# Kernel optimization log

Hardware: AMD Instinct MI355X
Metric: run time of the kernel (lower is better)

The kernel has to match this reference:

```python
import jax, jax.numpy as jnp
import numpy as np

B, T, C = 2, 2048, 1024
N_HEAD = 16
HEAD_DIM = C // N_HEAD  # 64


def _apply_rope(x, inv_freq):
    # x: [B, H, T, hd]. Matches the torch module's mixed RoPE variant:
    # cos/sin built from cat(freqs, freqs) but x split by even/odd strides.
    Tn, hd = x.shape[2], x.shape[3]
    t = jnp.arange(Tn, dtype=inv_freq.dtype)
    freqs = t[:, None] * inv_freq[None, :]            # [T, hd/2]
    emb = jnp.concatenate([freqs, freqs], axis=-1)    # [T, hd]
    cos = jnp.cos(emb)[None, None, :, :]
    sin = jnp.sin(emb)[None, None, :, :]
    x1 = x[..., 0::2]
    x2 = x[..., 1::2]
    # interleave (-x2, x1) back to last dim: stack then flatten last two dims
    x_rot = jnp.stack((-x2, x1), axis=-1).reshape(x.shape)
    return x * cos + x_rot * sin


def setup_inputs() -> dict:
    key = jax.random.key(0)
    k1, k2, k3 = jax.random.split(key, 3)
    x = jax.random.normal(k1, (B, T, C), dtype=jnp.float32)
    w_qkv = jax.random.normal(k2, (C, 3 * C), dtype=jnp.float32) * 0.02
    w_proj = jax.random.normal(k3, (C, C), dtype=jnp.float32) * 0.02
    return {"x": x, "w_qkv": w_qkv, "w_proj": w_proj}


def reference(x, w_qkv, w_proj):
    Bn, Tn, Cn = x.shape
    hd = HEAD_DIM
    inv_freq = 1.0 / (10000.0 ** (jnp.arange(0, hd, 2, dtype=jnp.float32) / hd))

    qkv = jnp.einsum('btc,cd->btd', x, w_qkv)  # [B, T, 3C]
    q, k, v = jnp.split(qkv, 3, axis=2)
    # [B, T, C] -> [B, H, T, hd]
    q = q.reshape(Bn, Tn, N_HEAD, hd).transpose(0, 2, 1, 3)
    k = k.reshape(Bn, Tn, N_HEAD, hd).transpose(0, 2, 1, 3)
    v = v.reshape(Bn, Tn, N_HEAD, hd).transpose(0, 2, 1, 3)

    q = _apply_rope(q, inv_freq)
    k = _apply_rope(k, inv_freq)

    scale = 1.0 / jnp.sqrt(jnp.asarray(hd, dtype=q.dtype))
    scores = jnp.einsum('bhqd,bhkd->bhqk', q, k) * scale  # [B, H, T, T]
    causal = jnp.tril(jnp.ones((Tn, Tn), dtype=bool))
    scores = jnp.where(causal[None, None, :, :], scores, -jnp.inf)
    attn = jax.nn.softmax(scores, axis=-1)
    out = jnp.einsum('bhqk,bhkd->bhqd', attn, v)          # [B, H, T, hd]
    y = out.transpose(0, 2, 1, 3).reshape(Bn, Tn, Cn)     # [B, T, C]
    return jnp.einsum('btc,cd->btd', y, w_proj)
```

## Files before the change

kernel.cpp:

```cpp
#include <hip/hip_runtime.h>
#include <hip/hip_bf16.h>

typedef unsigned short u16;
typedef unsigned int u32;
typedef __attribute__((ext_vector_type(8))) __bf16 bf16x8;
typedef __attribute__((ext_vector_type(4))) float f32x4;
typedef __attribute__((ext_vector_type(4))) u16 u16x4;
typedef __attribute__((ext_vector_type(4))) u32 u32x4;

__device__ __forceinline__ u16 f2bf(float f) {
  return __builtin_bit_cast(u16, (__bf16)f);
}
__device__ __forceinline__ float bf2f(u16 h) {
  return __builtin_bit_cast(float, (u32)h << 16);
}

__device__ __forceinline__ void gload_lds16(const void* g, void* l) {
  __builtin_amdgcn_global_load_lds((const __attribute__((address_space(1))) void*)g,
                                   (__attribute__((address_space(3))) void*)l, 16, 0, 0);
}

__global__ __launch_bounds__(256) void cvt_kernel(const float* __restrict__ in, u16* __restrict__ out) {
  const int i = (blockIdx.x * 256 + threadIdx.x) * 4;
  const float4 v = *(const float4*)(in + i);
  u16x4 r = {f2bf(v.x), f2bf(v.y), f2bf(v.z), f2bf(v.w)};
  *(u16x4*)(out + i) = r;
}

__global__ __launch_bounds__(256) void transpose_w(const float* __restrict__ w, u16* __restrict__ wt,
                                                   int K, int N) {
  __shared__ u16 tile[64][65];
  const int n0 = blockIdx.x * 64, k0 = blockIdx.y * 64;
  const int tid = threadIdx.x;
#pragma unroll
  for (int it = 0; it < 16; ++it) {
    const int idx = it * 256 + tid;
    const int r = idx >> 6, c = idx & 63;
    tile[r][c] = f2bf(w[(size_t)(k0 + r) * N + n0 + c]);
  }
  __syncthreads();
#pragma unroll
  for (int it = 0; it < 16; ++it) {
    const int idx = it * 256 + tid;
    const int r2 = idx >> 6, c2 = idx & 63;
    wt[(size_t)(n0 + r2) * K + k0 + c2] = tile[c2][r2];
  }
}

template <int BM, int OUT_F32>
__global__ __launch_bounds__(256) void gemm_bt(const u16* __restrict__ A, const u16* __restrict__ Bt,
                                               void* __restrict__ Cout, int M, int N, int K) {
  constexpr int MR = (BM == 128) ? 4 : 2;
  __shared__ u16 As[2][BM * 32];
  __shared__ u16 Bs[2][128 * 32];
  const int tid = threadIdx.x;
  const int wave = tid >> 6;
  const int lane = tid & 63;
  const int la = lane & 15, lb = lane >> 4;
  const int nwg = gridDim.x * gridDim.y;
  int lid = blockIdx.y * gridDim.x + blockIdx.x;
  lid = (lid & 7) * (nwg >> 3) + (lid >> 3);
  const int m0 = (lid % gridDim.x) * BM, n0 = (lid / gridDim.x) * 128;
  const int wr = (wave >> 1) * (BM / 2), wc = (wave & 1) * 64;
  const int srow = lane >> 2;
  const int scol = (lane & 3) * 8;
  const int c0 = wave * 2;

  auto stage = [&](int bb, int k0) {
    if (BM == 128) {
#pragma unroll
      for (int c2 = 0; c2 < 2; ++c2) {
        const int c = c0 + c2;
        const int row = c * 16 + srow;
        gload_lds16(A + (size_t)(m0 + row) * K + k0 + scol, As[bb] + c * 512);
      }
    } else {
      const int row = wave * 16 + srow;
      gload_lds16(A + (size_t)(m0 + row) * K + k0 + scol, As[bb] + wave * 512);
    }
#pragma unroll
    for (int c2 = 0; c2 < 2; ++c2) {
      const int c = c0 + c2;
      const int row = c * 16 + srow;
      gload_lds16(Bt + (size_t)(n0 + row) * K + k0 + scol, Bs[bb] + c * 512);
    }
  };

  f32x4 acc[MR][4] = {};
  const int nk = K >> 5;
  stage(0, 0);
  __syncthreads();
  int cur = 0;
  for (int t = 0; t < nk; ++t) {
    if (t + 1 < nk) stage(cur ^ 1, (t + 1) * 32);
    bf16x8 af[MR], bfr[4];
#pragma unroll
    for (int m = 0; m < MR; ++m) af[m] = *(const bf16x8*)&As[cur][(wr + m * 16 + la) * 32 + lb * 8];
#pragma unroll
    for (int n = 0; n < 4; ++n) bfr[n] = *(const bf16x8*)&Bs[cur][(wc + n * 16 + la) * 32 + lb * 8];
#pragma unroll
    for (int m = 0; m < MR; ++m)
#pragma unroll
      for (int n = 0; n < 4; ++n)
        acc[m][n] = __builtin_amdgcn_mfma_f32_16x16x32_bf16(af[m], bfr[n], acc[m][n], 0, 0, 0);
    __syncthreads();
    cur ^= 1;
  }
#pragma unroll
  for (int m = 0; m < MR; ++m)
#pragma unroll
    for (int n = 0; n < 4; ++n)
#pragma unroll
      for (int j = 0; j < 4; ++j) {
        const int row = m0 + wr + m * 16 + lb * 4 + j;
        const int col = n0 + wc + n * 16 + la;
        if (OUT_F32)
          ((float*)Cout)[(size_t)row * N + col] = acc[m][n][j];
        else
          ((u16*)Cout)[(size_t)row * N + col] = f2bf(acc[m][n][j]);
      }
}

__global__ __launch_bounds__(256) void rope_kernel(const u16* __restrict__ QKV, u16* __restrict__ Q,
                                                   u16* __restrict__ K, u16* __restrict__ Vt) {
  const int tt = blockIdx.x * 64;
  const int bh = blockIdx.y;
  const int b = bh >> 4, h = bh & 15;
  const int tid = threadIdx.x;
  __shared__ u16 vtile[64][65];
  const float NEG = -0.41524101186f;
  const float QSC = 0.18033688011f;

  const int i = tid & 31;
  const int d0 = 2 * i;
  const int j0 = d0 & 31, j1 = (d0 + 1) & 31;
  const float invf0 = exp2f(NEG * (float)j0);
  const float invf1 = exp2f(NEG * (float)j1);
  const int tl0 = tid >> 5;
  float s0, c0v, s1, c1v, sd0, cd0, sd1, cd1;
  sincosf((float)(tt + tl0) * invf0, &s0, &c0v);
  sincosf((float)(tt + tl0) * invf1, &s1, &c1v);
  sincosf(8.0f * invf0, &sd0, &cd0);
  sincosf(8.0f * invf1, &sd1, &cd1);

#pragma unroll
  for (int it = 0; it < 8; ++it) {
    const int t = tt + tl0 + it * 8;
    const size_t base = ((size_t)(b * 2048 + t)) * 3072 + h * 64 + d0;
    const size_t ob = ((size_t)bh * 2048 + t) * 64 + d0;
    {
      const float x0 = bf2f(QKV[base]), x1 = bf2f(QKV[base + 1]);
      const u32 lo = f2bf((x0 * c0v - x1 * s0) * QSC);
      const u32 hi = f2bf((x1 * c1v + x0 * s1) * QSC);
      *(u32*)(Q + ob) = lo | (hi << 16);
    }
    {
      const float x0 = bf2f(QKV[base + 1024]), x1 = bf2f(QKV[base + 1025]);
      const u32 lo = f2bf(x0 * c0v - x1 * s0);
      const u32 hi = f2bf(x1 * c1v + x0 * s1);
      *(u32*)(K + ob) = lo | (hi << 16);
    }
    const float nc0 = c0v * cd0 - s0 * sd0, ns0 = s0 * cd0 + c0v * sd0;
    c0v = nc0; s0 = ns0;
    const float nc1 = c1v * cd1 - s1 * sd1, ns1 = s1 * cd1 + c1v * sd1;
    c1v = nc1; s1 = ns1;
  }
#pragma unroll
  for (int it = 0; it < 8; ++it) {
    const int idx = it * 256 + tid;
    const int tl = idx >> 5, dd = (idx & 31) * 2;
    const size_t base = ((size_t)(b * 2048 + tt + tl)) * 3072 + 2048 + h * 64 + dd;
    vtile[tl][dd] = QKV[base];
    vtile[tl][dd + 1] = QKV[base + 1];
  }
  __syncthreads();
#pragma unroll
  for (int it = 0; it < 8; ++it) {
    const int idx = it * 256 + tid;
    const int dl = idx >> 5, tp = (idx & 31) * 2;
    const u32 val = (u32)vtile[tp][dl] | ((u32)vtile[tp + 1][dl] << 16);
    *(u32*)(Vt + ((size_t)bh * 64 + dl) * 2048 + tt + tp) = val;
  }
}

__global__ __launch_bounds__(256) void attn_kernel(const u16* __restrict__ Q, const u16* __restrict__ K,
                                                   const u16* __restrict__ Vt, u16* __restrict__ Y) {
  const int L = blockIdx.y * 32 + blockIdx.x;
  const int xcd = L & 7, slot = L >> 3;
  const int bh = xcd * 4 + (slot & 3);
  const int beta = 31 - (slot >> 2);
  const int b = bh >> 4, h = bh & 15;
  const int wave = threadIdx.x >> 6, lane = threadIdx.x & 63;
  const int la = lane & 15, lb = lane >> 4;
  const int q0 = beta * 64 + wave * 16;
  const int NT = beta + 1;

  __shared__ __align__(16) u16 KV[2][2][4096];

  const size_t plane = (size_t)bh * (2048 * 64);
  const char* Kb = (const char*)(K + plane);
  const char* Vb = (const char*)(Vt + plane);

  auto stage = [&](int buf, int kt) {
#pragma unroll
    for (int it = 0; it < 2; ++it) {
      const int ci = it * 256 + wave * 64 + lane;
      const int row = ci >> 3;
      const int cbs = ((ci & 7) * 16) ^ ((row & 7) << 4);
      const int n2 = row >> 4, rho = row & 15;
      const int srow = ((n2 & 1) << 5) + ((rho >> 2) << 3) + ((n2 >> 1) << 2) + (rho & 3);
      gload_lds16(Kb + (size_t)(kt * 64 + srow) * 128 + cbs,
                  (char*)&KV[buf][0][0] + it * 4096 + wave * 1024);
      gload_lds16(Vb + (size_t)row * 4096 + (size_t)kt * 128 + cbs,
                  (char*)&KV[buf][1][0] + it * 4096 + wave * 1024);
    }
  };

  stage(0, 0);

  bf16x8 qf[2];
#pragma unroll
  for (int s = 0; s < 2; ++s)
    qf[s] = *(const bf16x8*)(Q + plane + (size_t)(q0 + la) * 64 + s * 32 + lb * 8);

  f32x4 o[4] = {};
  float mreg = -1.0e30f;
  float plr = 0.f;

  const int x0 = (la & 7) << 4;
  const int cu0 = ((lb * 16) ^ x0) >> 1;
  const int cu1 = ((64 + lb * 16) ^ x0) >> 1;

  __syncthreads();
  int buf = 0;
  for (int kt = 0; kt < NT; ++kt) {
    if (kt + 1 < NT) stage(buf ^ 1, kt + 1);
    const u16* Kc = KV[buf][0];
    const u16* Vc = KV[buf][1];

    bf16x8 kf[2][4];
#pragma unroll
    for (int n = 0; n < 4; ++n) {
      kf[0][n] = *(const bf16x8*)&Kc[(n * 16 + la) * 64 + cu0];
      kf[1][n] = *(const bf16x8*)&Kc[(n * 16 + la) * 64 + cu1];
    }

    const int rowq = q0 + la;
    f32x4 sa[4] = {};
    __builtin_amdgcn_s_setprio(1);
#pragma unroll
    for (int s = 0; s < 2; ++s)
#pragma unroll
      for (int n = 0; n < 4; ++n)
        sa[n] = __builtin_amdgcn_mfma_f32_16x16x32_bf16(kf[s][n], qf[s], sa[n], 0, 0, 0);
    __builtin_amdgcn_s_setprio(0);
    if (kt == NT - 1) {
#pragma unroll
      for (int n = 0; n < 4; ++n)
#pragma unroll
        for (int j = 0; j < 4; ++j) {
          const int col = kt * 64 + ((n & 1) << 5) + (lb << 3) + ((n >> 1) << 2) + j;
          if (col > rowq) sa[n][j] = -1.0e30f;
        }
    }
    float mn_[4];
#pragma unroll
    for (int n = 0; n < 4; ++n)
      mn_[n] = fmaxf(fmaxf(sa[n][0], sa[n][1]), fmaxf(sa[n][2], sa[n][3]));
    const float lmax = fmaxf(fmaxf(mn_[0], mn_[1]), fmaxf(mn_[2], mn_[3]));
    if (__any(lmax > mreg + 8.0f)) {
      float v = fmaxf(lmax, __shfl_xor(lmax, 16));
      v = fmaxf(v, __shfl_xor(v, 32));
      const float mn = fmaxf(mreg, v);
      const float al = __builtin_amdgcn_exp2f(mreg - mn);
      plr *= al;
      mreg = mn;
      float alj[4];
#pragma unroll
      for (int j = 0; j < 4; ++j) alj[j] = __shfl(al, lb * 4 + j);
#pragma unroll
      for (int n = 0; n < 4; ++n)
#pragma unroll
        for (int j = 0; j < 4; ++j) o[n][j] *= alj[j];
    }
    u32 w[4][2];
    float ps = 0.f;
#pragma unroll
    for (int n = 0; n < 4; ++n) {
      const float p0 = __builtin_amdgcn_exp2f(sa[n][0] - mreg);
      const float p1 = __builtin_amdgcn_exp2f(sa[n][1] - mreg);
      const float p2 = __builtin_amdgcn_exp2f(sa[n][2] - mreg);
      const float p3 = __builtin_amdgcn_exp2f(sa[n][3] - mreg);
      ps += (p0 + p1) + (p2 + p3);
      w[n][0] = (u32)f2bf(p0) | ((u32)f2bf(p1) << 16);
      w[n][1] = (u32)f2bf(p2) | ((u32)f2bf(p3) << 16);
    }
    plr += ps;
    bf16x8 paf[2];
    paf[0] = __builtin_bit_cast(bf16x8, (u32x4){w[0][0], w[0][1], w[2][0], w[2][1]});
    paf[1] = __builtin_bit_cast(bf16x8, (u32x4){w[1][0], w[1][1], w[3][0], w[3][1]});

    bf16x8 vf[2][4];
#pragma unroll
    for (int n = 0; n < 4; ++n) {
      vf[0][n] = *(const bf16x8*)&Vc[(n * 16 + la) * 64 + cu0];
      vf[1][n] = *(const bf16x8*)&Vc[(n * 16 + la) * 64 + cu1];
    }
    __builtin_amdgcn_s_setprio(1);
#pragma unroll
    for (int n = 0; n < 4; ++n)
#pragma unroll
      for (int s = 0; s < 2; ++s)
        o[n] = __builtin_amdgcn_mfma_f32_16x16x32_bf16(paf[s], vf[s][n], o[n], 0, 0, 0);
    __builtin_amdgcn_s_setprio(0);

    __syncthreads();
    buf ^= 1;
  }

  float ls = plr;
  ls += __shfl_xor(ls, 16);
  ls += __shfl_xor(ls, 32);
  const float rinv = __builtin_amdgcn_rcpf(ls);
  float rj[4];
#pragma unroll
  for (int j = 0; j < 4; ++j) rj[j] = __shfl(rinv, lb * 4 + j);
#pragma unroll
  for (int n = 0; n < 4; ++n)
#pragma unroll
    for (int j = 0; j < 4; ++j) {
      const int t = q0 + lb * 4 + j;
      const int c = h * 64 + n * 16 + la;
      Y[((size_t)b * 2048 + t) * 1024 + c] = f2bf(o[n][j] * rj[j]);
    }
}

extern "C" void kernel_launch(void* const* d_in, const int* in_sizes, int n_in, void* d_out,
                              int out_size, void* d_ws, size_t ws_size, hipStream_t stream) {
  (void)in_sizes; (void)n_in; (void)out_size; (void)ws_size;
  const float* x = (const float*)d_in[0];
  const float* w_qkv = (const float*)d_in[1];
  const float* w_proj = (const float*)d_in[2];
  char* ws = (char*)d_ws;
  u16* xb     = (u16*)(ws);
  u16* wqkvT  = (u16*)(ws + 8388608);
  u16* wprojT = (u16*)(ws + 14680064);
  u16* qkv    = (u16*)(ws + 16777216);
  u16* q      = (u16*)(ws + 41943040);
  u16* k      = (u16*)(ws + 50331648);
  u16* vt     = (u16*)(ws + 58720256);
  u16* y      = xb;

  cvt_kernel<<<dim3(4096), dim3(256), 0, stream>>>(x, xb);
  transpose_w<<<dim3(48, 16), dim3(256), 0, stream>>>(w_qkv, wqkvT, 1024, 3072);
  transpose_w<<<dim3(16, 16), dim3(256), 0, stream>>>(w_proj, wprojT, 1024, 1024);
  gemm_bt<128, 0><<<dim3(32, 24), dim3(256), 0, stream>>>(xb, wqkvT, (void*)qkv, 4096, 3072, 1024);
  rope_kernel<<<dim3(32, 32), dim3(256), 0, stream>>>(qkv, q, k, vt);
  attn_kernel<<<dim3(32, 32), dim3(256), 0, stream>>>(q, k, vt, y);
  gemm_bt<64, 1><<<dim3(64, 8), dim3(256), 0, stream>>>(y, wprojT, d_out, 4096, 1024, 1024);
}
```

Measured before the change: 116.1 us.

## Split long causal attention bands across KV halves and merge three prep kernels

```diff
diff --git a/kernel.cpp b/kernel.cpp
--- a/kernel.cpp
+++ b/kernel.cpp
@@ -20,18 +20,31 @@
                                    (__attribute__((address_space(3))) void*)l, 16, 0, 0);
 }
 
-__global__ __launch_bounds__(256) void cvt_kernel(const float* __restrict__ in, u16* __restrict__ out) {
-  const int i = (blockIdx.x * 256 + threadIdx.x) * 4;
-  const float4 v = *(const float4*)(in + i);
-  u16x4 r = {f2bf(v.x), f2bf(v.y), f2bf(v.z), f2bf(v.w)};
-  *(u16x4*)(out + i) = r;
-}
-
-__global__ __launch_bounds__(256) void transpose_w(const float* __restrict__ w, u16* __restrict__ wt,
-                                                   int K, int N) {
+__global__ __launch_bounds__(256) void prep_kernel(const float* __restrict__ x, u16* __restrict__ xb,
+                                                   const float* __restrict__ wq, u16* __restrict__ wqT,
+                                                   const float* __restrict__ wp, u16* __restrict__ wpT) {
+  const int bid = blockIdx.x;
+  const int tid = threadIdx.x;
+  if (bid < 4096) {
+    const int i = (bid * 256 + tid) * 4;
+    const float4 v = *(const float4*)(x + i);
+    u16x4 r = {f2bf(v.x), f2bf(v.y), f2bf(v.z), f2bf(v.w)};
+    *(u16x4*)(xb + i) = r;
+    return;
+  }
   __shared__ u16 tile[64][65];
-  const int n0 = blockIdx.x * 64, k0 = blockIdx.y * 64;
-  const int tid = threadIdx.x;
+  const float* w;
+  u16* wt;
+  int K, N, n0, k0;
+  if (bid < 4864) {
+    const int id = bid - 4096;
+    w = wq; wt = wqT; K = 1024; N = 3072;
+    n0 = (id % 48) * 64; k0 = (id / 48) * 64;
+  } else {
+    const int id = bid - 4864;
+    w = wp; wt = wpT; K = 1024; N = 1024;
+    n0 = (id % 16) * 64; k0 = (id / 16) * 64;
+  }
 #pragma unroll
   for (int it = 0; it < 16; ++it) {
     const int idx = it * 256 + tid;
@@ -184,16 +197,21 @@
 }
 
 __global__ __launch_bounds__(256) void attn_kernel(const u16* __restrict__ Q, const u16* __restrict__ K,
-                                                   const u16* __restrict__ Vt, u16* __restrict__ Y) {
-  const int L = blockIdx.y * 32 + blockIdx.x;
-  const int xcd = L & 7, slot = L >> 3;
-  const int bh = xcd * 4 + (slot & 3);
-  const int beta = 31 - (slot >> 2);
+                                                   const u16* __restrict__ Vt, u16* __restrict__ Y,
+                                                   float* __restrict__ Part) {
+  const int L = blockIdx.x;
+  const int xcd = L & 7;
+  const int u = L >> 3;
+  const int bh = xcd * 4 + (u & 3);
+  const int c = u >> 2;
+  int band, kv0, nt;
+  if (c < 16)      { band = 31 - c; kv0 = 0;  nt = 16; }
+  else if (c < 32) { band = 47 - c; kv0 = 16; nt = band - 15; }
+  else             { band = 47 - c; kv0 = 0;  nt = band + 1; }
   const int b = bh >> 4, h = bh & 15;
   const int wave = threadIdx.x >> 6, lane = threadIdx.x & 63;
   const int la = lane & 15, lb = lane >> 4;
-  const int q0 = beta * 64 + wave * 16;
-  const int NT = beta + 1;
+  const int q0 = band * 64 + wave * 16;
 
   __shared__ __align__(16) u16 KV[2][2][4096];
 
@@ -201,7 +219,7 @@
   const char* Kb = (const char*)(K + plane);
   const char* Vb = (const char*)(Vt + plane);
 
-  auto stage = [&](int buf, int kt) {
+  auto stage = [&](int buf, int ktg) {
 #pragma unroll
     for (int it = 0; it < 2; ++it) {
       const int ci = it * 256 + wave * 64 + lane;
@@ -209,14 +227,14 @@
       const int cbs = ((ci & 7) * 16) ^ ((row & 7) << 4);
       const int n2 = row >> 4, rho = row & 15;
       const int srow = ((n2 & 1) << 5) + ((rho >> 2) << 3) + ((n2 >> 1) << 2) + (rho & 3);
-      gload_lds16(Kb + (size_t)(kt * 64 + srow) * 128 + cbs,
+      gload_lds16(Kb + (size_t)(ktg * 64 + srow) * 128 + cbs,
                   (char*)&KV[buf][0][0] + it * 4096 + wave * 1024);
-      gload_lds16(Vb + (size_t)row * 4096 + (size_t)kt * 128 + cbs,
+      gload_lds16(Vb + (size_t)row * 4096 + (size_t)ktg * 128 + cbs,
                   (char*)&KV[buf][1][0] + it * 4096 + wave * 1024);
     }
   };
 
-  stage(0, 0);
+  stage(0, kv0);
 
   bf16x8 qf[2];
 #pragma unroll
@@ -233,8 +251,9 @@
 
   __syncthreads();
   int buf = 0;
-  for (int kt = 0; kt < NT; ++kt) {
-    if (kt + 1 < NT) stage(buf ^ 1, kt + 1);
+  for (int kt = 0; kt < nt; ++kt) {
+    const int ktg = kv0 + kt;
+    if (kt + 1 < nt) stage(buf ^ 1, ktg + 1);
     const u16* Kc = KV[buf][0];
     const u16* Vc = KV[buf][1];
 
@@ -254,12 +273,12 @@
       for (int n = 0; n < 4; ++n)
         sa[n] = __builtin_amdgcn_mfma_f32_16x16x32_bf16(kf[s][n], qf[s], sa[n], 0, 0, 0);
     __builtin_amdgcn_s_setprio(0);
-    if (kt == NT - 1) {
+    if (ktg == band) {
 #pragma unroll
       for (int n = 0; n < 4; ++n)
 #pragma unroll
         for (int j = 0; j < 4; ++j) {
-          const int col = kt * 64 + ((n & 1) << 5) + (lb << 3) + ((n >> 1) << 2) + j;
+          const int col = ktg * 64 + ((n & 1) << 5) + (lb << 3) + ((n >> 1) << 2) + j;
           if (col > rowq) sa[n][j] = -1.0e30f;
         }
     }
@@ -321,18 +340,59 @@
   float ls = plr;
   ls += __shfl_xor(ls, 16);
   ls += __shfl_xor(ls, 32);
-  const float rinv = __builtin_amdgcn_rcpf(ls);
-  float rj[4];
-#pragma unroll
-  for (int j = 0; j < 4; ++j) rj[j] = __shfl(rinv, lb * 4 + j);
-#pragma unroll
-  for (int n = 0; n < 4; ++n)
-#pragma unroll
-    for (int j = 0; j < 4; ++j) {
-      const int t = q0 + lb * 4 + j;
-      const int c = h * 64 + n * 16 + la;
-      Y[((size_t)b * 2048 + t) * 1024 + c] = f2bf(o[n][j] * rj[j]);
-    }
+  if (c < 32) {
+    float* op = Part + (size_t)((bh * 16 + (band - 16)) * 2 + (kv0 ? 1 : 0)) * 4352;
+#pragma unroll
+    for (int n = 0; n < 4; ++n)
+#pragma unroll
+      for (int j = 0; j < 4; ++j)
+        op[(wave * 16 + lb * 4 + j) * 64 + n * 16 + la] = o[n][j];
+    if (lb == 0) {
+      op[4096 + wave * 16 + la] = mreg;
+      op[4160 + wave * 16 + la] = ls;
+    }
+  } else {
+    const float rinv = __builtin_amdgcn_rcpf(ls);
+    float rj[4];
+#pragma unroll
+    for (int j = 0; j < 4; ++j) rj[j] = __shfl(rinv, lb * 4 + j);
+#pragma unroll
+    for (int n = 0; n < 4; ++n)
+#pragma unroll
+      for (int j = 0; j < 4; ++j) {
+        const int t = q0 + lb * 4 + j;
+        const int cc = h * 64 + n * 16 + la;
+        Y[((size_t)b * 2048 + t) * 1024 + cc] = f2bf(o[n][j] * rj[j]);
+      }
+  }
+}
+
+__global__ __launch_bounds__(256) void attn_combine(const float* __restrict__ Part, u16* __restrict__ Y) {
+  const int g = blockIdx.x;
+  const int bh = g >> 4;
+  const int band = (g & 15) + 16;
+  const int b = bh >> 4, h = bh & 15;
+  const float* p0 = Part + (size_t)(g * 2) * 4352;
+  const float* p1 = p0 + 4352;
+  const int tid = threadIdx.x;
+  const int r = tid >> 2;
+  const int c0 = (tid & 3) * 16;
+  const float m0 = p0[4096 + r], l0 = p0[4160 + r];
+  const float m1 = p1[4096 + r], l1 = p1[4160 + r];
+  const float mx = fmaxf(m0, m1);
+  const float a0 = exp2f(m0 - mx), a1 = exp2f(m1 - mx);
+  const float rinv = 1.0f / (l0 * a0 + l1 * a1);
+  const int t = band * 64 + r;
+  u16* yr = Y + ((size_t)b * 2048 + t) * 1024 + h * 64 + c0;
+#pragma unroll
+  for (int q = 0; q < 4; ++q) {
+    const f32x4 v0 = *(const f32x4*)(p0 + r * 64 + c0 + q * 4);
+    const f32x4 v1 = *(const f32x4*)(p1 + r * 64 + c0 + q * 4);
+    u16x4 out;
+#pragma unroll
+    for (int e = 0; e < 4; ++e) out[e] = f2bf((v0[e] * a0 + v1[e] * a1) * rinv);
+    *(u16x4*)(yr + q * 4) = out;
+  }
 }
 
 extern "C" void kernel_launch(void* const* d_in, const int* in_sizes, int n_in, void* d_out,
@@ -350,12 +410,12 @@
   u16* k      = (u16*)(ws + 50331648);
   u16* vt     = (u16*)(ws + 58720256);
   u16* y      = xb;
-
-  cvt_kernel<<<dim3(4096), dim3(256), 0, stream>>>(x, xb);
-  transpose_w<<<dim3(48, 16), dim3(256), 0, stream>>>(w_qkv, wqkvT, 1024, 3072);
-  transpose_w<<<dim3(16, 16), dim3(256), 0, stream>>>(w_proj, wprojT, 1024, 1024);
+  float* part = (float*)qkv;
+
+  prep_kernel<<<dim3(5120), dim3(256), 0, stream>>>(x, xb, w_qkv, wqkvT, w_proj, wprojT);
   gemm_bt<128, 0><<<dim3(32, 24), dim3(256), 0, stream>>>(xb, wqkvT, (void*)qkv, 4096, 3072, 1024);
   rope_kernel<<<dim3(32, 32), dim3(256), 0, stream>>>(qkv, q, k, vt);
-  attn_kernel<<<dim3(32, 32), dim3(256), 0, stream>>>(q, k, vt, y);
+  attn_kernel<<<dim3(1536), dim3(256), 0, stream>>>(q, k, vt, y, part);
+  attn_combine<<<dim3(512), dim3(256), 0, stream>>>(part, y);
   gemm_bt<64, 1><<<dim3(64, 8), dim3(256), 0, stream>>>(y, wprojT, d_out, 4096, 1024, 1024);
 }
```

Result: no change. 117.4 us (+1.1%).

## Fuse RoPE and V transpose into QKV GEMM epilogue; merge prep kernels

Applied to the files above, without the earlier changes.

```diff
diff --git a/kernel.cpp b/kernel.cpp
--- a/kernel.cpp
+++ b/kernel.cpp
@@ -11,27 +11,37 @@
 __device__ __forceinline__ u16 f2bf(float f) {
   return __builtin_bit_cast(u16, (__bf16)f);
 }
-__device__ __forceinline__ float bf2f(u16 h) {
-  return __builtin_bit_cast(float, (u32)h << 16);
-}
 
 __device__ __forceinline__ void gload_lds16(const void* g, void* l) {
   __builtin_amdgcn_global_load_lds((const __attribute__((address_space(1))) void*)g,
                                    (__attribute__((address_space(3))) void*)l, 16, 0, 0);
 }
 
-__global__ __launch_bounds__(256) void cvt_kernel(const float* __restrict__ in, u16* __restrict__ out) {
-  const int i = (blockIdx.x * 256 + threadIdx.x) * 4;
-  const float4 v = *(const float4*)(in + i);
-  u16x4 r = {f2bf(v.x), f2bf(v.y), f2bf(v.z), f2bf(v.w)};
-  *(u16x4*)(out + i) = r;
-}
-
-__global__ __launch_bounds__(256) void transpose_w(const float* __restrict__ w, u16* __restrict__ wt,
-                                                   int K, int N) {
+__global__ __launch_bounds__(256) void prep_kernel(const float* __restrict__ x, u16* __restrict__ xb,
+                                                   const float* __restrict__ wq, u16* __restrict__ wqT,
+                                                   const float* __restrict__ wp, u16* __restrict__ wpT) {
+  const int bid = blockIdx.x;
+  const int tid = threadIdx.x;
+  if (bid < 4096) {
+    const int i = (bid * 256 + tid) * 4;
+    const float4 v = *(const float4*)(x + i);
+    u16x4 r = {f2bf(v.x), f2bf(v.y), f2bf(v.z), f2bf(v.w)};
+    *(u16x4*)(xb + i) = r;
+    return;
+  }
   __shared__ u16 tile[64][65];
-  const int n0 = blockIdx.x * 64, k0 = blockIdx.y * 64;
-  const int tid = threadIdx.x;
+  const float* w;
+  u16* wt;
+  int K, N, n0, k0;
+  if (bid < 4864) {
+    const int id = bid - 4096;
+    w = wq; wt = wqT; K = 1024; N = 3072;
+    n0 = (id % 48) * 64; k0 = (id / 48) * 64;
+  } else {
+    const int id = bid - 4864;
+    w = wp; wt = wpT; K = 1024; N = 1024;
+    n0 = (id % 16) * 64; k0 = (id / 16) * 64;
+  }
 #pragma unroll
   for (int it = 0; it < 16; ++it) {
     const int idx = it * 256 + tid;
@@ -47,9 +57,11 @@
   }
 }
 
-template <int BM, int OUT_F32>
+template <int BM, int MODE>
 __global__ __launch_bounds__(256) void gemm_bt(const u16* __restrict__ A, const u16* __restrict__ Bt,
-                                               void* __restrict__ Cout, int M, int N, int K) {
+                                               void* __restrict__ Cout, int M, int N, int K,
+                                               u16* __restrict__ Qo, u16* __restrict__ Ko,
+                                               u16* __restrict__ Vto) {
   constexpr int MR = (BM == 128) ? 4 : 2;
   __shared__ u16 As[2][BM * 32];
   __shared__ u16 Bs[2][128 * 32];
@@ -106,6 +118,60 @@
     __syncthreads();
     cur ^= 1;
   }
+
+  if (MODE == 2) {
+    const float NEG = -0.41524101186f;
+    const float QSC = 0.18033688011f;
+#pragma unroll
+    for (int n = 0; n < 4; ++n) {
+      const int c = n0 + wc + n * 16 + la;
+      const int d = c & 63;
+      const int h = (c & 1023) >> 6;
+      const int reg = c >> 10;
+      if (reg == 2) {
+#pragma unroll
+        for (int m = 0; m < MR; ++m) {
+          const int t0 = m0 + wr + m * 16 + lb * 4;
+          const int bb = t0 >> 11, tl0 = t0 & 2047;
+          u16x4 pv;
+#pragma unroll
+          for (int j = 0; j < 4; ++j) pv[j] = f2bf(acc[m][n][j]);
+          *(u16x4*)(Vto + ((size_t)(bb * 16 + h) * 64 + d) * 2048 + tl0) = pv;
+        }
+      } else {
+        const float invf = exp2f(NEG * (float)(d & 31));
+        const float sgn = (d & 1) ? 1.0f : -1.0f;
+        float s1, c1, s16, c16;
+        sincosf(invf, &s1, &c1);
+        sincosf(16.0f * invf, &s16, &c16);
+        const int tb = m0 + wr + lb * 4;
+        const int bb = tb >> 11;
+        const int tlb = tb & 2047;
+        const size_t plane = (size_t)(bb * 16 + h) * 2048;
+        float sm, cm;
+        sincosf((float)tlb * invf, &sm, &cm);
+        u16* dst = (reg == 0) ? Qo : Ko;
+        const float qs = (reg == 0) ? QSC : 1.0f;
+#pragma unroll
+        for (int m = 0; m < MR; ++m) {
+          float cj = cm, sj = sm;
+#pragma unroll
+          for (int j = 0; j < 4; ++j) {
+            const float val = acc[m][n][j];
+            const float prt = __shfl_xor(val, 1);
+            const float out = (val * cj + sgn * prt * sj) * qs;
+            dst[(plane + tlb + m * 16 + j) * 64 + d] = f2bf(out);
+            const float cn = cj * c1 - sj * s1, sn = sj * c1 + cj * s1;
+            cj = cn; sj = sn;
+          }
+          const float cn = cm * c16 - sm * s16, sn = sm * c16 + cm * s16;
+          cm = cn; sm = sn;
+        }
+      }
+    }
+    return;
+  }
+
 #pragma unroll
   for (int m = 0; m < MR; ++m)
 #pragma unroll
@@ -114,73 +180,11 @@
       for (int j = 0; j < 4; ++j) {
         const int row = m0 + wr + m * 16 + lb * 4 + j;
         const int col = n0 + wc + n * 16 + la;
-        if (OUT_F32)
+        if (MODE == 1)
           ((float*)Cout)[(size_t)row * N + col] = acc[m][n][j];
         else
           ((u16*)Cout)[(size_t)row * N + col] = f2bf(acc[m][n][j]);
       }
-}
-
-__global__ __launch_bounds__(256) void rope_kernel(const u16* __restrict__ QKV, u16* __restrict__ Q,
-                                                   u16* __restrict__ K, u16* __restrict__ Vt) {
-  const int tt = blockIdx.x * 64;
-  const int bh = blockIdx.y;
-  const int b = bh >> 4, h = bh & 15;
-  const int tid = threadIdx.x;
-  __shared__ u16 vtile[64][65];
-  const float NEG = -0.41524101186f;
-  const float QSC = 0.18033688011f;
-
-  const int i = tid & 31;
-  const int d0 = 2 * i;
-  const int j0 = d0 & 31, j1 = (d0 + 1) & 31;
-  const float invf0 = exp2f(NEG * (float)j0);
-  const float invf1 = exp2f(NEG * (float)j1);
-  const int tl0 = tid >> 5;
-  float s0, c0v, s1, c1v, sd0, cd0, sd1, cd1;
-  sincosf((float)(tt + tl0) * invf0, &s0, &c0v);
-  sincosf((float)(tt + tl0) * invf1, &s1, &c1v);
-  sincosf(8.0f * invf0, &sd0, &cd0);
-  sincosf(8.0f * invf1, &sd1, &cd1);
-
-#pragma unroll
-  for (int it = 0; it < 8; ++it) {
-    const int t = tt + tl0 + it * 8;
-    const size_t base = ((size_t)(b * 2048 + t)) * 3072 + h * 64 + d0;
-    const size_t ob = ((size_t)bh * 2048 + t) * 64 + d0;
-    {
-      const float x0 = bf2f(QKV[base]), x1 = bf2f(QKV[base + 1]);
-      const u32 lo = f2bf((x0 * c0v - x1 * s0) * QSC);
-      const u32 hi = f2bf((x1 * c1v + x0 * s1) * QSC);
-      *(u32*)(Q + ob) = lo | (hi << 16);
-    }
-    {
-      const float x0 = bf2f(QKV[base + 1024]), x1 = bf2f(QKV[base + 1025]);
-      const u32 lo = f2bf(x0 * c0v - x1 * s0);
-      const u32 hi = f2bf(x1 * c1v + x0 * s1);
-      *(u32*)(K + ob) = lo | (hi << 16);
-    }
-    const float nc0 = c0v * cd0 - s0 * sd0, ns0 = s0 * cd0 + c0v * sd0;
-    c0v = nc0; s0 = ns0;
-    const float nc1 = c1v * cd1 - s1 * sd1, ns1 = s1 * cd1 + c1v * sd1;
-    c1v = nc1; s1 = ns1;
-  }
-#pragma unroll
-  for (int it = 0; it < 8; ++it) {
-    const int idx = it * 256 + tid;
-    const int tl = idx >> 5, dd = (idx & 31) * 2;
-    const size_t base = ((size_t)(b * 2048 + tt + tl)) * 3072 + 2048 + h * 64 + dd;
-    vtile[tl][dd] = QKV[base];
-    vtile[tl][dd + 1] = QKV[base + 1];
-  }
-  __syncthreads();
-#pragma unroll
-  for (int it = 0; it < 8; ++it) {
-    const int idx = it * 256 + tid;
-    const int dl = idx >> 5, tp = (idx & 31) * 2;
-    const u32 val = (u32)vtile[tp][dl] | ((u32)vtile[tp + 1][dl] << 16);
-    *(u32*)(Vt + ((size_t)bh * 64 + dl) * 2048 + tt + tp) = val;
-  }
 }
 
 __global__ __launch_bounds__(256) void attn_kernel(const u16* __restrict__ Q, const u16* __restrict__ K,
@@ -345,17 +349,15 @@
   u16* xb     = (u16*)(ws);
   u16* wqkvT  = (u16*)(ws + 8388608);
   u16* wprojT = (u16*)(ws + 14680064);
-  u16* qkv    = (u16*)(ws + 16777216);
-  u16* q      = (u16*)(ws + 41943040);
-  u16* k      = (u16*)(ws + 50331648);
-  u16* vt     = (u16*)(ws + 58720256);
+  u16* q      = (u16*)(ws + 16777216);
+  u16* k      = (u16*)(ws + 25165824);
+  u16* vt     = (u16*)(ws + 33554432);
   u16* y      = xb;
 
-  cvt_kernel<<<dim3(4096), dim3(256), 0, stream>>>(x, xb);
-  transpose_w<<<dim3(48, 16), dim3(256), 0, stream>>>(w_qkv, wqkvT, 1024, 3072);
-  transpose_w<<<dim3(16, 16), dim3(256), 0, stream>>>(w_proj, wprojT, 1024, 1024);
-  gemm_bt<128, 0><<<dim3(32, 24), dim3(256), 0, stream>>>(xb, wqkvT, (void*)qkv, 4096, 3072, 1024);
-  rope_kernel<<<dim3(32, 32), dim3(256), 0, stream>>>(qkv, q, k, vt);
+  prep_kernel<<<dim3(5120), dim3(256), 0, stream>>>(x, xb, w_qkv, wqkvT, w_proj, wprojT);
+  gemm_bt<128, 2><<<dim3(32, 24), dim3(256), 0, stream>>>(xb, wqkvT, nullptr, 4096, 3072, 1024,
+                                                          q, k, vt);
   attn_kernel<<<dim3(32, 32), dim3(256), 0, stream>>>(q, k, vt, y);
-  gemm_bt<64, 1><<<dim3(64, 8), dim3(256), 0, stream>>>(y, wprojT, d_out, 4096, 1024, 1024);
-}
+  gemm_bt<64, 1><<<dim3(64, 8), dim3(256), 0, stream>>>(y, wprojT, d_out, 4096, 1024, 1024,
+                                                        nullptr, nullptr, nullptr);
+}
```

Result: faster. 106.4 us (median of 2 runs) (-8.3%).
